# Optimization experiments

Hardware: AMD Instinct MI355X
Metric: run time of the kernel (lower is better)

Reference implementation:

```python
import jax, jax.numpy as jnp
import numpy as np

B, N, D, A = 4, 2048, 1024, 256


def setup_inputs() -> dict:
    key = jax.random.key(0)
    k1, k2, k3, k4, k5 = jax.random.split(key, 5)
    s = 1.0 / np.sqrt(D)
    return {
        "inputs": jax.random.normal(k1, (B, N, D), dtype=jnp.float32),
        "attention_mask": jnp.zeros((B, 1, N), dtype=jnp.float32),
        "Wq": jax.random.normal(k2, (D, A), dtype=jnp.float32) * s,
        "bq": jax.random.normal(k3, (A,), dtype=jnp.float32) * 0.01,
        "Wk": jax.random.normal(k4, (D, A), dtype=jnp.float32) * s,
        "bk": jax.random.normal(k5, (A,), dtype=jnp.float32) * 0.01,
    }


def reference(inputs, attention_mask, Wq, bq, Wk, bk):
    # q, k: [B, N, A]; v = inputs: [B, N, D]
    q = jnp.einsum('bnd,da->bna', inputs, Wq) + bq
    k = jnp.einsum('bnd,da->bna', inputs, Wk) + bk
    # unscaled scores, faithful to source (no 1/sqrt(d))
    scores = jnp.einsum('bna,bma->bnm', q, k) + attention_mask  # [B, N, N]
    probs = jax.nn.softmax(scores, axis=-1)
    # dropout is identity in eval mode
    context = jnp.einsum('bnm,bmd->bnd', probs, inputs)  # [B, N, D]
    return context
```

## Files before the change

kernel.cpp:

```cpp
#include <hip/hip_runtime.h>
#include <hip/hip_bf16.h>


#define BB 4
#define NN 2048
#define DD 1024
#define AA 256

using bf16x8 = __attribute__((ext_vector_type(8))) __bf16;
using f32x4  = __attribute__((ext_vector_type(4))) float;

#define MFMA(a, b, c) __builtin_amdgcn_mfma_f32_16x16x32_bf16(a, b, c, 0, 0, 0)

#define VMCNT(n) asm volatile("s_waitcnt vmcnt(" #n ")" ::: "memory")
#define CFENCE() asm volatile("" ::: "memory")
#define BARRIER() __builtin_amdgcn_s_barrier()

static __device__ __forceinline__ unsigned short f2bf(float x) {
    union { float f; unsigned int u; } c; c.f = x;
    unsigned int u = c.u;
    u += 0x7fffu + ((u >> 16) & 1u);
    return (unsigned short)(u >> 16);
}
static __device__ __forceinline__ float bf2f(unsigned short h) {
    union { unsigned int u; float f; } c; c.u = ((unsigned int)h) << 16;
    return c.f;
}

template<int SLOTS>
static __device__ __forceinline__ int swz(int r) {
    return (SLOTS == 4) ? ((r >> 1) & 3) : (r & 7);
}

template<int ROWS, int BK, int THREADS, int I0, int I1>
static __device__ __forceinline__ void stage_part(const unsigned short* __restrict__ g,
                                                  int pitch, unsigned short* lds, int t) {
    constexpr int SLOTS = BK / 8;
#pragma unroll
    for (int i = I0; i < I1; ++i) {
        int tt = t + i * THREADS;
        int row = tt / SLOTS;
        int slot = (tt % SLOTS) ^ swz<SLOTS>(row);
        const char* src = (const char*)(g + (size_t)row * pitch) + slot * 16;
        __builtin_amdgcn_global_load_lds((const unsigned int*)src,
                                         (unsigned int*)((char*)lds + (size_t)tt * 16),
                                         16, 0, 0);
    }
}

template<int BK>
static __device__ __forceinline__ bf16x8 ldsfrag(const unsigned short* lds, int row,
                                                 int ks, int lane) {
    constexpr int SLOTS = BK / 8;
    int r = row + (lane & 15);
    int slot = (ks * 4 + (lane >> 4)) ^ swz<SLOTS>(r);
    return *reinterpret_cast<const bf16x8*>((const char*)lds + (size_t)r * (BK * 2) + slot * 16);
}

__global__ __launch_bounds__(256) void k_prep(const float* __restrict__ X,
                                              unsigned short* __restrict__ Xh,
                                              unsigned short* __restrict__ Xl,
                                              unsigned short* __restrict__ XT) {
    __shared__ unsigned short tile[64][65];
    int t = threadIdx.x;
    int n0 = blockIdx.x * 64, d0 = blockIdx.y * 64;
    const float* Xb = X + (size_t)blockIdx.z * NN * DD;
    unsigned short* Xhb = Xh + (size_t)blockIdx.z * NN * DD;
    unsigned short* Xlb = Xl + (size_t)blockIdx.z * NN * DD;
    unsigned short* XTb = XT + (size_t)blockIdx.z * DD * NN;
    int r = t >> 4, c4 = (t & 15) * 4;
#pragma unroll
    for (int i = 0; i < 4; ++i) {
        int row = r + 16 * i;
        float4 v = *reinterpret_cast<const float4*>(Xb + (size_t)(n0 + row) * DD + d0 + c4);
        ushort4 h, l;
        h.x = f2bf(v.x); l.x = f2bf(v.x - bf2f(h.x));
        h.y = f2bf(v.y); l.y = f2bf(v.y - bf2f(h.y));
        h.z = f2bf(v.z); l.z = f2bf(v.z - bf2f(h.z));
        h.w = f2bf(v.w); l.w = f2bf(v.w - bf2f(h.w));
        *reinterpret_cast<ushort4*>(Xhb + (size_t)(n0 + row) * DD + d0 + c4) = h;
        *reinterpret_cast<ushort4*>(Xlb + (size_t)(n0 + row) * DD + d0 + c4) = l;
        tile[c4 + 0][row] = h.x;
        tile[c4 + 1][row] = h.y;
        tile[c4 + 2][row] = h.z;
        tile[c4 + 3][row] = h.w;
    }
    __syncthreads();
    int j = t & 63, i4 = t >> 6;
#pragma unroll
    for (int jj = i4; jj < 64; jj += 4)
        XTb[(size_t)(d0 + jj) * NN + n0 + j] = tile[jj][j];
}

__global__ __launch_bounds__(256) void k_wsplit(const float* __restrict__ W,
                                                unsigned short* __restrict__ WTh,
                                                unsigned short* __restrict__ WTl) {
    int idx = blockIdx.x * 256 + threadIdx.x;
    int a = idx >> 10;
    int d = idx & (DD - 1);
    float w = W[(size_t)d * AA + a];
    unsigned short hi = f2bf(w);
    WTh[idx] = hi;
    WTl[idx] = f2bf(w - bf2f(hi));
}

__global__ __launch_bounds__(256) void k_proj(const unsigned short* __restrict__ Xh,
                                              const unsigned short* __restrict__ Xl,
                                              const unsigned short* __restrict__ WqTh,
                                              const unsigned short* __restrict__ WqTl,
                                              const unsigned short* __restrict__ WkTh,
                                              const unsigned short* __restrict__ WkTl,
                                              const float* __restrict__ bq,
                                              const float* __restrict__ bk,
                                              unsigned short* __restrict__ Qh,
                                              unsigned short* __restrict__ Ql,
                                              unsigned short* __restrict__ Kh,
                                              unsigned short* __restrict__ Kl) {
    __shared__ unsigned short ldsAh[2][64 * 32], ldsAl[2][64 * 32];
    __shared__ unsigned short ldsBh[2][128 * 32], ldsBl[2][128 * 32];
    int t = threadIdx.x, lane = t & 63, wave = t >> 6;
    int row0 = blockIdx.x * 64;
    int which = blockIdx.y >> 1;
    int col0 = (blockIdx.y & 1) * 128;
    const unsigned short* BTh = which ? WkTh : WqTh;
    const unsigned short* BTl = which ? WkTl : WqTl;
    const float* bias = which ? bk : bq;
    unsigned short* Oh = which ? Kh : Qh;
    unsigned short* Ol = which ? Kl : Ql;
    const unsigned short* Abase_h = Xh + (size_t)row0 * DD;
    const unsigned short* Abase_l = Xl + (size_t)row0 * DD;
    const unsigned short* Bbase_h = BTh + (size_t)col0 * DD;
    const unsigned short* Bbase_l = BTl + (size_t)col0 * DD;
    int wc = wave * 32;
    f32x4 acc[4][2] = {};
    stage_part<64, 32, 256, 0, 1>(Abase_h, DD, ldsAh[0], t);
    stage_part<64, 32, 256, 0, 1>(Abase_l, DD, ldsAl[0], t);
    stage_part<128, 32, 256, 0, 2>(Bbase_h, DD, ldsBh[0], t);
    stage_part<128, 32, 256, 0, 2>(Bbase_l, DD, ldsBl[0], t);
    constexpr int NT = DD / 32;
    for (int tt = 0; tt < NT; ++tt) {
        int cur = tt & 1;
        CFENCE();
        BARRIER();
        if (tt + 1 < NT) {
            int k0 = (tt + 1) * 32;
            stage_part<64, 32, 256, 0, 1>(Abase_h + k0, DD, ldsAh[cur ^ 1], t);
            stage_part<64, 32, 256, 0, 1>(Abase_l + k0, DD, ldsAl[cur ^ 1], t);
            stage_part<128, 32, 256, 0, 2>(Bbase_h + k0, DD, ldsBh[cur ^ 1], t);
            stage_part<128, 32, 256, 0, 2>(Bbase_l + k0, DD, ldsBl[cur ^ 1], t);
            VMCNT(6);
        } else {
            VMCNT(0);
        }
        BARRIER();
        CFENCE();
        bf16x8 ah[4], al[4], bh[2], bl[2];
#pragma unroll
        for (int f = 0; f < 4; ++f) {
            ah[f] = ldsfrag<32>(ldsAh[cur], f * 16, 0, lane);
            al[f] = ldsfrag<32>(ldsAl[cur], f * 16, 0, lane);
        }
#pragma unroll
        for (int n = 0; n < 2; ++n) {
            bh[n] = ldsfrag<32>(ldsBh[cur], wc + n * 16, 0, lane);
            bl[n] = ldsfrag<32>(ldsBl[cur], wc + n * 16, 0, lane);
        }
        __builtin_amdgcn_s_setprio(1);
#pragma unroll
        for (int m = 0; m < 4; ++m)
#pragma unroll
            for (int n = 0; n < 2; ++n) {
                acc[m][n] = MFMA(ah[m], bh[n], acc[m][n]);
                acc[m][n] = MFMA(ah[m], bl[n], acc[m][n]);
                acc[m][n] = MFMA(al[m], bh[n], acc[m][n]);
            }
        __builtin_amdgcn_s_setprio(0);
    }
    int r4 = (lane >> 4) << 2, cl = lane & 15;
#pragma unroll
    for (int m = 0; m < 4; ++m)
#pragma unroll
        for (int n = 0; n < 2; ++n) {
            int col = col0 + wc + n * 16 + cl;
            float bv = bias[col];
#pragma unroll
            for (int r = 0; r < 4; ++r) {
                int row = row0 + m * 16 + r4 + r;
                float v = acc[m][n][r] + bv;
                unsigned short hi = f2bf(v);
                size_t o = (size_t)row * AA + col;
                Oh[o] = hi;
                Ol[o] = f2bf(v - bf2f(hi));
            }
        }
}

__global__ __launch_bounds__(256) void k_scores(const unsigned short* __restrict__ Qh,
                                                const unsigned short* __restrict__ Ql,
                                                const unsigned short* __restrict__ Kh,
                                                const unsigned short* __restrict__ Kl,
                                                float* __restrict__ S) {
    __shared__ unsigned short ldsAh[2][128 * 32], ldsAl[2][128 * 32];
    __shared__ unsigned short ldsBh[2][128 * 32], ldsBl[2][128 * 32];
    int t = threadIdx.x, lane = t & 63, wave = t >> 6;
    int b = blockIdx.z;
    int nrow0 = blockIdx.x * 128;
    int mcol0 = blockIdx.y * 128;
    const unsigned short* Qhb = Qh + (size_t)(b * NN + nrow0) * AA;
    const unsigned short* Qlb = Ql + (size_t)(b * NN + nrow0) * AA;
    const unsigned short* Khb = Kh + (size_t)(b * NN + mcol0) * AA;
    const unsigned short* Klb = Kl + (size_t)(b * NN + mcol0) * AA;
    int wr = (wave >> 1) * 64, wc = (wave & 1) * 64;
    f32x4 acc[4][4] = {};
    stage_part<128, 32, 256, 0, 2>(Qhb, AA, ldsAh[0], t);
    stage_part<128, 32, 256, 0, 2>(Qlb, AA, ldsAl[0], t);
    stage_part<128, 32, 256, 0, 2>(Khb, AA, ldsBh[0], t);
    stage_part<128, 32, 256, 0, 2>(Klb, AA, ldsBl[0], t);
    constexpr int NT = AA / 32;
    for (int tt = 0; tt < NT; ++tt) {
        int cur = tt & 1;
        CFENCE();
        BARRIER();
        if (tt + 1 < NT) {
            int k0 = (tt + 1) * 32;
            stage_part<128, 32, 256, 0, 2>(Qhb + k0, AA, ldsAh[cur ^ 1], t);
            stage_part<128, 32, 256, 0, 2>(Qlb + k0, AA, ldsAl[cur ^ 1], t);
            stage_part<128, 32, 256, 0, 2>(Khb + k0, AA, ldsBh[cur ^ 1], t);
            stage_part<128, 32, 256, 0, 2>(Klb + k0, AA, ldsBl[cur ^ 1], t);
            VMCNT(8);
        } else {
            VMCNT(0);
        }
        BARRIER();
        CFENCE();
        bf16x8 ah[4], al[4], bh[4], bl[4];
#pragma unroll
        for (int f = 0; f < 4; ++f) {
            ah[f] = ldsfrag<32>(ldsAh[cur], wr + f * 16, 0, lane);
            al[f] = ldsfrag<32>(ldsAl[cur], wr + f * 16, 0, lane);
            bh[f] = ldsfrag<32>(ldsBh[cur], wc + f * 16, 0, lane);
            bl[f] = ldsfrag<32>(ldsBl[cur], wc + f * 16, 0, lane);
        }
        __builtin_amdgcn_s_setprio(1);
#pragma unroll
        for (int m = 0; m < 4; ++m)
#pragma unroll
            for (int n = 0; n < 4; ++n) {
                acc[m][n] = MFMA(ah[m], bh[n], acc[m][n]);
                acc[m][n] = MFMA(ah[m], bl[n], acc[m][n]);
                acc[m][n] = MFMA(al[m], bh[n], acc[m][n]);
            }
        __builtin_amdgcn_s_setprio(0);
    }
    int r4 = (lane >> 4) << 2, cl = lane & 15;
#pragma unroll
    for (int m = 0; m < 4; ++m)
#pragma unroll
        for (int n = 0; n < 4; ++n) {
#pragma unroll
            for (int r = 0; r < 4; ++r) {
                int nrow = nrow0 + wr + m * 16 + r4 + r;
                int mcol = mcol0 + wc + n * 16 + cl;
                S[((size_t)(b * NN + nrow)) * NN + mcol] = acc[m][n][r];
            }
        }
}

__global__ __launch_bounds__(256) void k_softmax(float* __restrict__ S,
                                                 const float* __restrict__ mask) {
    int row = blockIdx.x;
    int b = row >> 11;
    float* srow = S + (size_t)row * NN;
    const float4* S4 = (const float4*)srow;
    const float4* M4 = (const float4*)(mask + (size_t)b * NN);
    int t = threadIdx.x;
    float4 a0 = S4[t], a1 = S4[t + 256];
    float4 m0 = M4[t], m1 = M4[t + 256];
    float v[8];
    v[0] = a0.x + m0.x; v[1] = a0.y + m0.y; v[2] = a0.z + m0.z; v[3] = a0.w + m0.w;
    v[4] = a1.x + m1.x; v[5] = a1.y + m1.y; v[6] = a1.z + m1.z; v[7] = a1.w + m1.w;
    float mx = v[0];
#pragma unroll
    for (int i = 1; i < 8; ++i) mx = fmaxf(mx, v[i]);
#pragma unroll
    for (int off = 32; off; off >>= 1) mx = fmaxf(mx, __shfl_xor(mx, off));
    __shared__ float redm[4], reds[4];
    int lane = t & 63, wave = t >> 6;
    if (lane == 0) redm[wave] = mx;
    __syncthreads();
    mx = fmaxf(fmaxf(redm[0], redm[1]), fmaxf(redm[2], redm[3]));
    float s = 0.f;
#pragma unroll
    for (int i = 0; i < 8; ++i) { v[i] = __expf(v[i] - mx); s += v[i]; }
#pragma unroll
    for (int off = 32; off; off >>= 1) s += __shfl_xor(s, off);
    if (lane == 0) reds[wave] = s;
    __syncthreads();
    s = reds[0] + reds[1] + reds[2] + reds[3];
    float inv = 1.0f / s;
    ushort4 w0, w1;
    w0.x = f2bf(v[0] * inv); w0.y = f2bf(v[1] * inv);
    w0.z = f2bf(v[2] * inv); w0.w = f2bf(v[3] * inv);
    w1.x = f2bf(v[4] * inv); w1.y = f2bf(v[5] * inv);
    w1.z = f2bf(v[6] * inv); w1.w = f2bf(v[7] * inv);
    ushort4* prow4 = (ushort4*)srow;
    prow4[t] = w0;
    prow4[t + 256] = w1;
}

__global__ __launch_bounds__(512, 2) void k_pv(const float* __restrict__ Sbuf,
                                               const unsigned short* __restrict__ XT,
                                               float* __restrict__ Out) {
    extern __shared__ unsigned short dyn[];
    int t = threadIdx.x, lane = t & 63, wave = t >> 6;
    int wm = wave >> 2, wn = wave & 3;
    int bid = blockIdx.x + 16 * (blockIdx.y + 4 * blockIdx.z);
    int sbid = (bid & 7) * 32 + (bid >> 3);
    int bx = sbid & 15;
    int by = (sbid >> 4) & 3;
    int b = sbid >> 6;
    int nrow0 = bx * 128, d0 = by * 256;
    const unsigned short* Pb = (const unsigned short*)Sbuf + (size_t)(b * NN + nrow0) * (NN * 2);
    const unsigned short* XTb = XT + (size_t)b * DD * NN + (size_t)d0 * NN;
    f32x4 acc[4][4] = {};
    stage_part<128, 64, 512, 0, 2>(Pb, NN * 2, dyn, t);
    stage_part<256, 64, 512, 0, 4>(XTb, NN, dyn + 24576, t);
    stage_part<128, 64, 512, 0, 2>(Pb + 64, NN * 2, dyn + 8192, t);
    stage_part<256, 64, 512, 0, 4>(XTb + 64, NN, dyn + 24576 + 16384, t);
    constexpr int NT = NN / 64;
    int cur = 0;
    for (int kt = 0; kt < NT; ++kt) {
        int st = (cur >= 1) ? cur - 1 : 2;
        const unsigned short* An = Pb + (kt + 2) * 64;
        const unsigned short* Bn = XTb + (kt + 2) * 64;
        bool pf = (kt + 2 < NT);
        CFENCE();
        BARRIER();
        if (kt == NT - 1) { VMCNT(0); } else { VMCNT(6); }
        CFENCE();
        const unsigned short* A = dyn + cur * 8192;
        const unsigned short* Bt = dyn + 24576 + cur * 16384;
        unsigned short* Ast = dyn + st * 8192;
        unsigned short* Bst = dyn + 24576 + st * 16384;
#pragma unroll
        for (int p = 0; p < 4; ++p) {
            int mq = p >> 1, nq = p & 1;
            if (pf) {
                if (p == 0)      stage_part<128, 64, 512, 0, 2>(An, NN * 2, Ast, t);
                else if (p == 1) stage_part<256, 64, 512, 0, 2>(Bn, NN, Bst, t);
                else if (p == 2) stage_part<256, 64, 512, 2, 4>(Bn, NN, Bst, t);
            }
            bf16x8 pa[2][2], vb[2][2];
#pragma unroll
            for (int m = 0; m < 2; ++m)
#pragma unroll
                for (int ks = 0; ks < 2; ++ks)
                    pa[m][ks] = ldsfrag<64>(A, wm * 64 + mq * 32 + m * 16, ks, lane);
#pragma unroll
            for (int n = 0; n < 2; ++n)
#pragma unroll
                for (int ks = 0; ks < 2; ++ks)
                    vb[n][ks] = ldsfrag<64>(Bt, wn * 64 + nq * 32 + n * 16, ks, lane);
            __builtin_amdgcn_s_setprio(1);
#pragma unroll
            for (int ks = 0; ks < 2; ++ks)
#pragma unroll
                for (int m = 0; m < 2; ++m)
#pragma unroll
                    for (int n = 0; n < 2; ++n)
                        acc[mq * 2 + m][nq * 2 + n] =
                            MFMA(pa[m][ks], vb[n][ks], acc[mq * 2 + m][nq * 2 + n]);
            __builtin_amdgcn_s_setprio(0);
        }
        cur = (cur == 2) ? 0 : cur + 1;
    }
    int r4 = (lane >> 4) << 2, cl = lane & 15;
#pragma unroll
    for (int mi = 0; mi < 4; ++mi)
#pragma unroll
        for (int ni = 0; ni < 4; ++ni) {
#pragma unroll
            for (int r = 0; r < 4; ++r) {
                int row = b * NN + nrow0 + wm * 64 + mi * 16 + r4 + r;
                int dc = d0 + wn * 64 + ni * 16 + cl;
                Out[(size_t)row * DD + dc] = acc[mi][ni][r];
            }
        }
}

extern "C" void kernel_launch(void* const* d_in, const int* in_sizes, int n_in,
                              void* d_out, int out_size, void* d_ws, size_t ws_size,
                              hipStream_t stream) {
    const float* X    = (const float*)d_in[0];
    const float* mask = (const float*)d_in[1];
    const float* Wq   = (const float*)d_in[2];
    const float* bq   = (const float*)d_in[3];
    const float* Wk   = (const float*)d_in[4];
    const float* bk   = (const float*)d_in[5];
    float* Out = (float*)d_out;

    unsigned short* Xh   = (unsigned short*)d_ws;
    unsigned short* Xl   = Xh + (size_t)BB * NN * DD;
    unsigned short* XT   = Xl + (size_t)BB * NN * DD;
    unsigned short* WqTh = XT + (size_t)BB * NN * DD;
    unsigned short* WqTl = WqTh + (size_t)AA * DD;
    unsigned short* WkTh = WqTl + (size_t)AA * DD;
    unsigned short* WkTl = WkTh + (size_t)AA * DD;
    unsigned short* Qh   = WkTl + (size_t)AA * DD;
    unsigned short* Ql   = Qh + (size_t)BB * NN * AA;
    unsigned short* Kh   = Ql + (size_t)BB * NN * AA;
    unsigned short* Kl   = Kh + (size_t)BB * NN * AA;
    float* S = (float*)(Kl + (size_t)BB * NN * AA);

    hipFuncSetAttribute((const void*)k_pv,
                        hipFuncAttributeMaxDynamicSharedMemorySize, 147456);

    k_prep<<<dim3(NN / 64, DD / 64, BB), 256, 0, stream>>>(X, Xh, Xl, XT);
    k_wsplit<<<dim3((AA * DD) / 256), 256, 0, stream>>>(Wq, WqTh, WqTl);
    k_wsplit<<<dim3((AA * DD) / 256), 256, 0, stream>>>(Wk, WkTh, WkTl);

    k_proj<<<dim3((BB * NN) / 64, 4), 256, 0, stream>>>(Xh, Xl, WqTh, WqTl, WkTh, WkTl,
                                                        bq, bk, Qh, Ql, Kh, Kl);

    k_scores<<<dim3(NN / 128, NN / 128, BB), 256, 0, stream>>>(Qh, Ql, Kh, Kl, S);
    k_softmax<<<dim3(BB * NN), 256, 0, stream>>>(S, mask);
    k_pv<<<dim3(16, 4, BB), 512, 147456, stream>>>(S, XT, Out);
}
```

Baseline: 153.4 us.

## Remap blocks across XCDs and restructure pipeline waits in proj, scores, pv

Block IDs for k_proj and k_scores are remapped with an XCD-aware swizzle, so blocks that share operands land on the same chiplet and reuse its L2. The double-buffered loops now wait for all outstanding loads before one barrier, then issue the next prefetch, instead of waiting on partial counts with two barriers. k_pv stages its full tile at once, loads all LDS fragments up front behind an lgkmcnt wait and scheduling barrier, then issues all MFMAs in one batch. This cuts barriers and interleaving overhead, but VMCNT(0) at the top may expose global-load latency that was previously overlapped.

```diff
diff --git a/kernel.cpp b/kernel.cpp
--- a/kernel.cpp
+++ b/kernel.cpp
@@ -13,6 +13,8 @@
 #define MFMA(a, b, c) __builtin_amdgcn_mfma_f32_16x16x32_bf16(a, b, c, 0, 0, 0)
 
 #define VMCNT(n) asm volatile("s_waitcnt vmcnt(" #n ")" ::: "memory")
+#define LGKM0()  asm volatile("s_waitcnt lgkmcnt(0)" ::: "memory")
+#define SB0()    __builtin_amdgcn_sched_barrier(0)
 #define CFENCE() asm volatile("" ::: "memory")
 #define BARRIER() __builtin_amdgcn_s_barrier()
 
@@ -119,9 +121,12 @@
     __shared__ unsigned short ldsAh[2][64 * 32], ldsAl[2][64 * 32];
     __shared__ unsigned short ldsBh[2][128 * 32], ldsBl[2][128 * 32];
     int t = threadIdx.x, lane = t & 63, wave = t >> 6;
-    int row0 = blockIdx.x * 64;
-    int which = blockIdx.y >> 1;
-    int col0 = (blockIdx.y & 1) * 128;
+    int bid = blockIdx.x;
+    int sbid = (bid & 7) * 64 + (bid >> 3);
+    int row0 = (sbid & 127) * 64;
+    int yy = sbid >> 7;
+    int which = yy >> 1;
+    int col0 = (yy & 1) * 128;
     const unsigned short* BTh = which ? WkTh : WqTh;
     const unsigned short* BTl = which ? WkTl : WqTl;
     const float* bias = which ? bk : bq;
@@ -141,19 +146,16 @@
     for (int tt = 0; tt < NT; ++tt) {
         int cur = tt & 1;
         CFENCE();
+        VMCNT(0);
         BARRIER();
+        CFENCE();
         if (tt + 1 < NT) {
             int k0 = (tt + 1) * 32;
             stage_part<64, 32, 256, 0, 1>(Abase_h + k0, DD, ldsAh[cur ^ 1], t);
             stage_part<64, 32, 256, 0, 1>(Abase_l + k0, DD, ldsAl[cur ^ 1], t);
             stage_part<128, 32, 256, 0, 2>(Bbase_h + k0, DD, ldsBh[cur ^ 1], t);
             stage_part<128, 32, 256, 0, 2>(Bbase_l + k0, DD, ldsBl[cur ^ 1], t);
-            VMCNT(6);
-        } else {
-            VMCNT(0);
-        }
-        BARRIER();
-        CFENCE();
+        }
         bf16x8 ah[4], al[4], bh[2], bl[2];
 #pragma unroll
         for (int f = 0; f < 4; ++f) {
@@ -165,6 +167,8 @@
             bh[n] = ldsfrag<32>(ldsBh[cur], wc + n * 16, 0, lane);
             bl[n] = ldsfrag<32>(ldsBl[cur], wc + n * 16, 0, lane);
         }
+        LGKM0();
+        SB0();
         __builtin_amdgcn_s_setprio(1);
 #pragma unroll
         for (int m = 0; m < 4; ++m)
@@ -203,9 +207,11 @@
     __shared__ unsigned short ldsAh[2][128 * 32], ldsAl[2][128 * 32];
     __shared__ unsigned short ldsBh[2][128 * 32], ldsBl[2][128 * 32];
     int t = threadIdx.x, lane = t & 63, wave = t >> 6;
-    int b = blockIdx.z;
-    int nrow0 = blockIdx.x * 128;
-    int mcol0 = blockIdx.y * 128;
+    int bid = blockIdx.x + 16 * blockIdx.y + 256 * blockIdx.z;
+    int sbid = (bid & 7) * 128 + (bid >> 3);
+    int b = sbid >> 8;
+    int nrow0 = (sbid & 15) * 128;
+    int mcol0 = ((sbid >> 4) & 15) * 128;
     const unsigned short* Qhb = Qh + (size_t)(b * NN + nrow0) * AA;
     const unsigned short* Qlb = Ql + (size_t)(b * NN + nrow0) * AA;
     const unsigned short* Khb = Kh + (size_t)(b * NN + mcol0) * AA;
@@ -220,19 +226,16 @@
     for (int tt = 0; tt < NT; ++tt) {
         int cur = tt & 1;
         CFENCE();
+        VMCNT(0);
         BARRIER();
+        CFENCE();
         if (tt + 1 < NT) {
             int k0 = (tt + 1) * 32;
             stage_part<128, 32, 256, 0, 2>(Qhb + k0, AA, ldsAh[cur ^ 1], t);
             stage_part<128, 32, 256, 0, 2>(Qlb + k0, AA, ldsAl[cur ^ 1], t);
             stage_part<128, 32, 256, 0, 2>(Khb + k0, AA, ldsBh[cur ^ 1], t);
             stage_part<128, 32, 256, 0, 2>(Klb + k0, AA, ldsBl[cur ^ 1], t);
-            VMCNT(8);
-        } else {
-            VMCNT(0);
-        }
-        BARRIER();
-        CFENCE();
+        }
         bf16x8 ah[4], al[4], bh[4], bl[4];
 #pragma unroll
         for (int f = 0; f < 4; ++f) {
@@ -241,6 +244,8 @@
             bh[f] = ldsfrag<32>(ldsBh[cur], wc + f * 16, 0, lane);
             bl[f] = ldsfrag<32>(ldsBl[cur], wc + f * 16, 0, lane);
         }
+        LGKM0();
+        SB0();
         __builtin_amdgcn_s_setprio(1);
 #pragma unroll
         for (int m = 0; m < 4; ++m)
@@ -331,47 +336,38 @@
     int cur = 0;
     for (int kt = 0; kt < NT; ++kt) {
         int st = (cur >= 1) ? cur - 1 : 2;
-        const unsigned short* An = Pb + (kt + 2) * 64;
-        const unsigned short* Bn = XTb + (kt + 2) * 64;
-        bool pf = (kt + 2 < NT);
-        CFENCE();
+        CFENCE();
+        if (kt == NT - 1) { VMCNT(0); } else { VMCNT(6); }
         BARRIER();
-        if (kt == NT - 1) { VMCNT(0); } else { VMCNT(6); }
-        CFENCE();
-        const unsigned short* A = dyn + cur * 8192;
+        CFENCE();
+        const unsigned short* A  = dyn + cur * 8192;
         const unsigned short* Bt = dyn + 24576 + cur * 16384;
-        unsigned short* Ast = dyn + st * 8192;
-        unsigned short* Bst = dyn + 24576 + st * 16384;
-#pragma unroll
-        for (int p = 0; p < 4; ++p) {
-            int mq = p >> 1, nq = p & 1;
-            if (pf) {
-                if (p == 0)      stage_part<128, 64, 512, 0, 2>(An, NN * 2, Ast, t);
-                else if (p == 1) stage_part<256, 64, 512, 0, 2>(Bn, NN, Bst, t);
-                else if (p == 2) stage_part<256, 64, 512, 2, 4>(Bn, NN, Bst, t);
-            }
-            bf16x8 pa[2][2], vb[2][2];
-#pragma unroll
-            for (int m = 0; m < 2; ++m)
-#pragma unroll
-                for (int ks = 0; ks < 2; ++ks)
-                    pa[m][ks] = ldsfrag<64>(A, wm * 64 + mq * 32 + m * 16, ks, lane);
-#pragma unroll
-            for (int n = 0; n < 2; ++n)
-#pragma unroll
-                for (int ks = 0; ks < 2; ++ks)
-                    vb[n][ks] = ldsfrag<64>(Bt, wn * 64 + nq * 32 + n * 16, ks, lane);
-            __builtin_amdgcn_s_setprio(1);
+        if (kt + 2 < NT) {
+            stage_part<128, 64, 512, 0, 2>(Pb + (kt + 2) * 64, NN * 2, dyn + st * 8192, t);
+            stage_part<256, 64, 512, 0, 4>(XTb + (kt + 2) * 64, NN, dyn + 24576 + st * 16384, t);
+        }
+        bf16x8 pa[4][2], vb[4][2];
+#pragma unroll
+        for (int mi = 0; mi < 4; ++mi)
 #pragma unroll
             for (int ks = 0; ks < 2; ++ks)
-#pragma unroll
-                for (int m = 0; m < 2; ++m)
-#pragma unroll
-                    for (int n = 0; n < 2; ++n)
-                        acc[mq * 2 + m][nq * 2 + n] =
-                            MFMA(pa[m][ks], vb[n][ks], acc[mq * 2 + m][nq * 2 + n]);
-            __builtin_amdgcn_s_setprio(0);
-        }
+                pa[mi][ks] = ldsfrag<64>(A, wm * 64 + mi * 16, ks, lane);
+#pragma unroll
+        for (int ni = 0; ni < 4; ++ni)
+#pragma unroll
+            for (int ks = 0; ks < 2; ++ks)
+                vb[ni][ks] = ldsfrag<64>(Bt, wn * 64 + ni * 16, ks, lane);
+        LGKM0();
+        SB0();
+        __builtin_amdgcn_s_setprio(1);
+#pragma unroll
+        for (int ks = 0; ks < 2; ++ks)
+#pragma unroll
+            for (int mi = 0; mi < 4; ++mi)
+#pragma unroll
+                for (int ni = 0; ni < 4; ++ni)
+                    acc[mi][ni] = MFMA(pa[mi][ks], vb[ni][ks], acc[mi][ni]);
+        __builtin_amdgcn_s_setprio(0);
         cur = (cur == 2) ? 0 : cur + 1;
     }
     int r4 = (lane >> 4) << 2, cl = lane & 15;
@@ -419,8 +415,8 @@
     k_wsplit<<<dim3((AA * DD) / 256), 256, 0, stream>>>(Wq, WqTh, WqTl);
     k_wsplit<<<dim3((AA * DD) / 256), 256, 0, stream>>>(Wk, WkTh, WkTl);
 
-    k_proj<<<dim3((BB * NN) / 64, 4), 256, 0, stream>>>(Xh, Xl, WqTh, WqTl, WkTh, WkTl,
-                                                        bq, bk, Qh, Ql, Kh, Kl);
+    k_proj<<<dim3((BB * NN) / 64 * 4), 256, 0, stream>>>(Xh, Xl, WqTh, WqTl, WkTh, WkTl,
+                                                         bq, bk, Qh, Ql, Kh, Kl);
 
     k_scores<<<dim3(NN / 128, NN / 128, BB), 256, 0, stream>>>(Qh, Ql, Kh, Kl, S);
     k_softmax<<<dim3(BB * NN), 256, 0, stream>>>(S, mask);
```

After: 155.7 us. No clear change (+1.5%).
